# Kernel optimization log

Hardware: AMD Instinct MI355X
Metric: run time of the kernel (lower is better)

Reference implementation:

```python
import jax, jax.numpy as jnp
import numpy as np

# SOM hyperparameters (match init_kwargs)
M, N = 64, 64
NODES = M * N
FEATS = 256
BATCH = 1024
LR = 0.5
RADIUS_FACTOR = 1.1
TOTAL_ITER = 100000
SIGMA = max(M, N) * RADIUS_FACTOR


def setup_inputs() -> dict:
    key = jax.random.key(0)
    k1, k2 = jax.random.split(key)
    x = jax.random.uniform(k1, (BATCH, FEATS), dtype=jnp.float32)
    map_w = jax.random.uniform(k2, (NODES, FEATS), dtype=jnp.float32)
    return {"x": x, "map_w": map_w, "iteration": 0}


def _grid_locs():
    ii, jj = jnp.meshgrid(jnp.arange(M), jnp.arange(N), indexing='ij')
    return jnp.stack([ii.ravel(), jj.ravel()], axis=1)  # (NODES, 2) int32


def reference(x, map_w, iteration):
    B = x.shape[0]
    # ---- feedforward: squared distances (B, NODES) via GEMM expansion,
    # avoiding the (B, NODES, FEATS) broadcast the TF code materializes.
    x2 = jnp.sum(x * x, axis=1, keepdims=True)          # (B, 1)
    w2 = jnp.sum(map_w * map_w, axis=1)                  # (NODES,)
    sqd = x2 + w2[None, :] - 2.0 * (x @ map_w.T)         # (B, NODES)
    bmu_indices = jnp.argmin(sqd, axis=1)                # (B,)

    # ---- backprop: neighborhood-weighted codebook update
    locs = _grid_locs()                                  # (NODES, 2)
    bmu_locs = locs[bmu_indices]                         # (B, 2)
    # grid distance^2 between every node and each sample's BMU: (B, NODES)
    d2 = jnp.sum((locs[None, :, :] - bmu_locs[:, None, :]) ** 2, axis=2).astype(jnp.float32)

    lambda_g = TOTAL_ITER / SIGMA
    decay = jnp.exp(jnp.float32(-float(iteration) / lambda_g))
    radius = SIGMA * decay + 1e-6
    lr = LR * decay

    impact = jnp.exp(-d2 / (2.0 * radius * radius))
    in_radius = (jnp.sqrt(d2) <= radius).astype(jnp.float32)
    lr_op = impact * in_radius * lr                      # (B, NODES)

    # weight_update[n,d] = sum_b lr_op[b,n] * (x[b,d] - map_w[n,d])
    # computed without the (B, NODES, FEATS) intermediate:
    upd = (jnp.einsum('bn,bd->nd', lr_op, x) - lr_op.sum(axis=0)[:, None] * map_w) / B
    new_map = map_w + upd
    return new_map, bmu_indices
```

## Files before the change

kernel.cpp:

```cpp
#include <hip/hip_runtime.h>
#include <math.h>

#define NODES 4096
#define FEATS 256
#define BATCH 1024
#define LR_C 0.5f
#define SIGMA_C 70.4f

typedef _Float16 f16x8 __attribute__((ext_vector_type(8)));
typedef float floatx4 __attribute__((ext_vector_type(4)));

__device__ __forceinline__ void get_params(int it, float& lr, float& r2, float& i2r2) {
    float decay = __expf(-(float)it * (SIGMA_C / 100000.0f));
    float radius = SIGMA_C * decay + 1e-6f;
    lr = LR_C * decay;
    r2 = radius * radius;
    i2r2 = 1.0f / (2.0f * r2);
}

__device__ __forceinline__ unsigned fkey(float f) {
    unsigned u = __float_as_uint(f);
    return (u & 0x80000000u) ? ~u : (u | 0x80000000u);
}
__device__ __forceinline__ unsigned long long shfl_xor_u64(unsigned long long v, int mask) {
    unsigned lo = (unsigned)v, hi = (unsigned)(v >> 32);
    lo = __shfl_xor(lo, mask, 64);
    hi = __shfl_xor(hi, mask, 64);
    return ((unsigned long long)hi << 32) | lo;
}

__global__ __launch_bounds__(256) void k_gemm1min(const float* __restrict__ X, const float* __restrict__ Wm,
                                                  unsigned long long* __restrict__ gmin) {
    __shared__ _Float16 Ah[128][40];
    __shared__ _Float16 Al[128][40];
    __shared__ _Float16 Bh[64][40];
    __shared__ _Float16 Bl[64][40];
    __shared__ float w2s[64];
    const int n0 = blockIdx.x * 64;
    const int b0 = blockIdx.y * 128;
    const int t = threadIdx.x;
    const int wave = t >> 6, lane = t & 63;
    const int lm = lane & 15, quad = lane >> 4;
    const int arow = t >> 1, ako = (t & 1) * 16;
    const int brow = t >> 2, bko = (t & 3) * 8;
    float w2p = 0.0f;
    floatx4 acc[2][4] = {};
    for (int k0 = 0; k0 < FEATS; k0 += 32) {
        {
            union { _Float16 h[16]; float4 q[2]; } uh, ul;
#pragma unroll
            for (int c = 0; c < 4; ++c) {
                float4 v = *(const float4*)&X[(size_t)(b0 + arow) * FEATS + k0 + ako + c * 4];
                _Float16 h0 = (_Float16)v.x, h1 = (_Float16)v.y, h2 = (_Float16)v.z, h3 = (_Float16)v.w;
                uh.h[c * 4 + 0] = h0; uh.h[c * 4 + 1] = h1; uh.h[c * 4 + 2] = h2; uh.h[c * 4 + 3] = h3;
                ul.h[c * 4 + 0] = (_Float16)(v.x - (float)h0);
                ul.h[c * 4 + 1] = (_Float16)(v.y - (float)h1);
                ul.h[c * 4 + 2] = (_Float16)(v.z - (float)h2);
                ul.h[c * 4 + 3] = (_Float16)(v.w - (float)h3);
            }
            *(float4*)&Ah[arow][ako] = uh.q[0];
            *(float4*)&Ah[arow][ako + 8] = uh.q[1];
            *(float4*)&Al[arow][ako] = ul.q[0];
            *(float4*)&Al[arow][ako + 8] = ul.q[1];
        }
        {
            union { _Float16 h[8]; float4 q; } uh, ul;
#pragma unroll
            for (int c = 0; c < 2; ++c) {
                float4 v = *(const float4*)&Wm[(size_t)(n0 + brow) * FEATS + k0 + bko + c * 4];
                w2p += v.x * v.x + v.y * v.y + v.z * v.z + v.w * v.w;
                _Float16 h0 = (_Float16)v.x, h1 = (_Float16)v.y, h2 = (_Float16)v.z, h3 = (_Float16)v.w;
                uh.h[c * 4 + 0] = h0; uh.h[c * 4 + 1] = h1; uh.h[c * 4 + 2] = h2; uh.h[c * 4 + 3] = h3;
                ul.h[c * 4 + 0] = (_Float16)(v.x - (float)h0);
                ul.h[c * 4 + 1] = (_Float16)(v.y - (float)h1);
                ul.h[c * 4 + 2] = (_Float16)(v.z - (float)h2);
                ul.h[c * 4 + 3] = (_Float16)(v.w - (float)h3);
            }
            *(float4*)&Bh[brow][bko] = uh.q;
            *(float4*)&Bl[brow][bko] = ul.q;
        }
        __syncthreads();
        f16x8 ah[2], al[2], bh[4], bl[4];
#pragma unroll
        for (int i = 0; i < 2; ++i) {
            ah[i] = *(f16x8*)&Ah[wave * 32 + i * 16 + lm][quad * 8];
            al[i] = *(f16x8*)&Al[wave * 32 + i * 16 + lm][quad * 8];
        }
#pragma unroll
        for (int j = 0; j < 4; ++j) {
            bh[j] = *(f16x8*)&Bh[j * 16 + lm][quad * 8];
            bl[j] = *(f16x8*)&Bl[j * 16 + lm][quad * 8];
        }
#pragma unroll
        for (int i = 0; i < 2; ++i)
#pragma unroll
            for (int j = 0; j < 4; ++j) {
                acc[i][j] = __builtin_amdgcn_mfma_f32_16x16x32_f16(ah[i], bh[j], acc[i][j], 0, 0, 0);
                acc[i][j] = __builtin_amdgcn_mfma_f32_16x16x32_f16(ah[i], bl[j], acc[i][j], 0, 0, 0);
                acc[i][j] = __builtin_amdgcn_mfma_f32_16x16x32_f16(al[i], bh[j], acc[i][j], 0, 0, 0);
            }
        __syncthreads();
    }
    w2p += __shfl_xor(w2p, 1, 64);
    w2p += __shfl_xor(w2p, 2, 64);
    if ((t & 3) == 0) w2s[brow] = w2p;
    __syncthreads();
#pragma unroll
    for (int i = 0; i < 2; ++i)
#pragma unroll
        for (int r = 0; r < 4; ++r) {
            const int row = b0 + wave * 32 + i * 16 + quad * 4 + r;
            unsigned long long m = 0xFFFFFFFFFFFFFFFFULL;
#pragma unroll
            for (int j = 0; j < 4; ++j) {
                float v = w2s[j * 16 + lm] - 2.0f * acc[i][j][r];
                unsigned long long k = ((unsigned long long)fkey(v) << 32) | (unsigned)(n0 + j * 16 + lm);
                if (k < m) m = k;
            }
#pragma unroll
            for (int mk = 1; mk < 16; mk <<= 1) {
                unsigned long long o = shfl_xor_u64(m, mk);
                if (o < m) m = o;
            }
            if (lm == 0) atomicMin(&gmin[row], m);
        }
}

__global__ __launch_bounds__(256) void k_lropX(const unsigned long long* __restrict__ gmin,
                                               const int* __restrict__ itp, const float* __restrict__ X,
                                               _Float16* __restrict__ lrT, float* __restrict__ Svec,
                                               _Float16* __restrict__ XT, float* __restrict__ out1) {
    const int blk = blockIdx.x;
    const int t = threadIdx.x;
    if (blk < 2048) {
        __shared__ int bmu_s[1024];
        __shared__ float texp[64];
        __shared__ float red4[4];
#pragma unroll
        for (int j = 0; j < 4; ++j)
            bmu_s[t + j * 256] = (int)(gmin[t + j * 256] & 0xFFFFFFFFULL);
        float lr, r2, i2r2;
        get_params(itp[0], lr, r2, i2r2);
        if (t < 64) texp[t] = __expf(-(float)(t * t) * i2r2);
        __syncthreads();
        if (blk < 4) out1[blk * 256 + t] = (float)bmu_s[blk * 256 + t];
        const int n = blk * 2 + (t >> 7);
        const int b0 = (t & 127) * 8;
        const int ni = n >> 6, nj = n & 63;
        float s = 0.0f;
        union { _Float16 h[8]; float4 q; } u;
#pragma unroll
        for (int c = 0; c < 8; ++c) {
            int m = bmu_s[b0 + c];
            int di = ni - (m >> 6); di = di < 0 ? -di : di;
            int dj = nj - (m & 63); dj = dj < 0 ? -dj : dj;
            int d2 = di * di + dj * dj;
            float val = ((float)d2 <= r2) ? lr * texp[di] * texp[dj] : 0.0f;
            u.h[c] = (_Float16)val;
            s += val;
        }
        *(float4*)&lrT[(size_t)n * BATCH + b0] = u.q;
        const int lane = t & 63, wave = t >> 6;
#pragma unroll
        for (int off = 32; off > 0; off >>= 1) s += __shfl_down(s, off, 64);
        if (lane == 0) red4[wave] = s;
        __syncthreads();
        if (t < 2) Svec[blk * 2 + t] = red4[2 * t] + red4[2 * t + 1];
    } else {
        __shared__ _Float16 T[64][72];
        const int blk2 = blk - 2048;
        const int b0 = (blk2 & 15) * 64, d0 = (blk2 >> 4) * 64;
        {
            const int bl = t >> 2, dq = (t & 3) * 16;
            union { _Float16 h[16]; } u;
#pragma unroll
            for (int c = 0; c < 4; ++c) {
                float4 v = *(const float4*)&X[(size_t)(b0 + bl) * FEATS + d0 + dq + c * 4];
                u.h[c * 4 + 0] = (_Float16)v.x; u.h[c * 4 + 1] = (_Float16)v.y;
                u.h[c * 4 + 2] = (_Float16)v.z; u.h[c * 4 + 3] = (_Float16)v.w;
            }
#pragma unroll
            for (int c = 0; c < 16; ++c) T[bl][dq + c] = u.h[c];
        }
        __syncthreads();
        {
            const int dl = t >> 2, bq = (t & 3) * 16;
            union { _Float16 h[16]; float4 q[2]; } u;
#pragma unroll
            for (int c = 0; c < 16; ++c) u.h[c] = T[bq + c][dl];
            *(float4*)&XT[(size_t)(d0 + dl) * BATCH + b0 + bq] = u.q[0];
            *(float4*)&XT[(size_t)(d0 + dl) * BATCH + b0 + bq + 8] = u.q[1];
        }
    }
}

__global__ __launch_bounds__(256) void k_gemm2c(const _Float16* __restrict__ lrT, const _Float16* __restrict__ XT,
                                                const float* __restrict__ Svec, const float* __restrict__ Wm,
                                                float* __restrict__ out0) {
    __shared__ _Float16 As[32][136];
    __shared__ _Float16 Bs[64][136];
    __shared__ float Svl[32];
    const int d0 = blockIdx.x * 64;
    const int n0 = blockIdx.y * 32;
    const int t = threadIdx.x;
    const int wave = t >> 6, lane = t & 63;
    const int wm = wave & 1, wn = wave >> 1;
    const int lm = lane & 15, quad = lane >> 4;
    if (t < 32) Svl[t] = Svec[n0 + t];
    const int arow = t >> 3, acoff = (t & 7) * 16;
    const int brow = t >> 2, bcoff = (t & 3) * 32;
    floatx4 acc0 = {}, acc1 = {};
    for (int k0 = 0; k0 < BATCH; k0 += 128) {
        *(float4*)&As[arow][acoff] = *(const float4*)&lrT[(size_t)(n0 + arow) * BATCH + k0 + acoff];
        *(float4*)&As[arow][acoff + 8] = *(const float4*)&lrT[(size_t)(n0 + arow) * BATCH + k0 + acoff + 8];
#pragma unroll
        for (int c = 0; c < 4; ++c)
            *(float4*)&Bs[brow][bcoff + c * 8] =
                *(const float4*)&XT[(size_t)(d0 + brow) * BATCH + k0 + bcoff + c * 8];
        __syncthreads();
#pragma unroll
        for (int ks = 0; ks < 128; ks += 32) {
            f16x8 a = *(f16x8*)&As[wm * 16 + lm][ks + quad * 8];
            f16x8 b0 = *(f16x8*)&Bs[wn * 32 + lm][ks + quad * 8];
            f16x8 b1 = *(f16x8*)&Bs[wn * 32 + 16 + lm][ks + quad * 8];
            acc0 = __builtin_amdgcn_mfma_f32_16x16x32_f16(a, b0, acc0, 0, 0, 0);
            acc1 = __builtin_amdgcn_mfma_f32_16x16x32_f16(a, b1, acc1, 0, 0, 0);
        }
        __syncthreads();
    }
    const float invB = 1.0f / (float)BATCH;
#pragma unroll
    for (int r = 0; r < 4; ++r) {
        int rowN = n0 + wm * 16 + quad * 4 + r;
        float cc = 1.0f - Svl[rowN - n0] * invB;
        int col0 = d0 + wn * 32 + lm;
        int col1 = col0 + 16;
        out0[(size_t)rowN * FEATS + col0] = Wm[(size_t)rowN * FEATS + col0] * cc + acc0[r] * invB;
        out0[(size_t)rowN * FEATS + col1] = Wm[(size_t)rowN * FEATS + col1] * cc + acc1[r] * invB;
    }
}

extern "C" void kernel_launch(void* const* d_in, const int* in_sizes, int n_in,
                              void* d_out, int out_size, void* d_ws, size_t ws_size,
                              hipStream_t stream) {
    const float* X = (const float*)d_in[0];
    const float* Wm = (const float*)d_in[1];
    const int* itp = (const int*)d_in[2];
    float* out0 = (float*)d_out;
    float* out1 = out0 + (size_t)NODES * FEATS;

    char* ws = (char*)d_ws;
    unsigned long long* gmin = (unsigned long long*)(ws + 0);
    float* Svec     = (float*)(ws + 8192);
    _Float16* XT    = (_Float16*)(ws + 24576);
    _Float16* lrT   = (_Float16*)(ws + 548864);

    hipMemsetAsync(gmin, 0xFF, 1024 * sizeof(unsigned long long), stream);
    k_gemm1min<<<dim3(64, 8), 256, 0, stream>>>(X, Wm, gmin);
    k_lropX<<<2112, 256, 0, stream>>>(gmin, itp, X, lrT, Svec, XT, out1);
    k_gemm2c<<<dim3(4, 128), 256, 0, stream>>>(lrT, XT, Svec, Wm, out0);
}
```

Measured before the change: 96.53 us.

## Fuse lr_op generation into second GEMM and move X transpose into first kernel

```diff
diff --git a/kernel.cpp b/kernel.cpp
--- a/kernel.cpp
+++ b/kernel.cpp
@@ -30,15 +30,44 @@
 }
 
 __global__ __launch_bounds__(256) void k_gemm1min(const float* __restrict__ X, const float* __restrict__ Wm,
-                                                  unsigned long long* __restrict__ gmin) {
+                                                  unsigned long long* __restrict__ gmin,
+                                                  _Float16* __restrict__ XT) {
+    const int t = threadIdx.x;
+    const int blk = blockIdx.x;
+    if (blk >= 512) {
+        __shared__ _Float16 T[64][72];
+        const int blk2 = blk - 512;
+        const int b0 = (blk2 & 15) * 64, d0 = (blk2 >> 4) * 64;
+        {
+            const int bl = t >> 2, dq = (t & 3) * 16;
+            _Float16 h[16];
+#pragma unroll
+            for (int c = 0; c < 4; ++c) {
+                float4 v = *(const float4*)&X[(size_t)(b0 + bl) * FEATS + d0 + dq + c * 4];
+                h[c * 4 + 0] = (_Float16)v.x; h[c * 4 + 1] = (_Float16)v.y;
+                h[c * 4 + 2] = (_Float16)v.z; h[c * 4 + 3] = (_Float16)v.w;
+            }
+#pragma unroll
+            for (int c = 0; c < 16; ++c) T[bl][dq + c] = h[c];
+        }
+        __syncthreads();
+        {
+            const int dl = t >> 2, bq = (t & 3) * 16;
+            union { _Float16 h[16]; float4 q[2]; } u;
+#pragma unroll
+            for (int c = 0; c < 16; ++c) u.h[c] = T[bq + c][dl];
+            *(float4*)&XT[(size_t)(d0 + dl) * BATCH + b0 + bq] = u.q[0];
+            *(float4*)&XT[(size_t)(d0 + dl) * BATCH + b0 + bq + 8] = u.q[1];
+        }
+        return;
+    }
     __shared__ _Float16 Ah[128][40];
     __shared__ _Float16 Al[128][40];
     __shared__ _Float16 Bh[64][40];
     __shared__ _Float16 Bl[64][40];
     __shared__ float w2s[64];
-    const int n0 = blockIdx.x * 64;
-    const int b0 = blockIdx.y * 128;
-    const int t = threadIdx.x;
+    const int n0 = (blk & 63) * 64;
+    const int b0 = (blk >> 6) * 128;
     const int wave = t >> 6, lane = t & 63;
     const int lm = lane & 15, quad = lane >> 4;
     const int arow = t >> 1, ako = (t & 1) * 16;
@@ -126,117 +155,82 @@
         }
 }
 
-__global__ __launch_bounds__(256) void k_lropX(const unsigned long long* __restrict__ gmin,
-                                               const int* __restrict__ itp, const float* __restrict__ X,
-                                               _Float16* __restrict__ lrT, float* __restrict__ Svec,
-                                               _Float16* __restrict__ XT, float* __restrict__ out1) {
+__global__ __launch_bounds__(256) void k_gemm2d(const unsigned long long* __restrict__ gmin,
+                                                const int* __restrict__ itp,
+                                                const _Float16* __restrict__ XT,
+                                                const float* __restrict__ Wm,
+                                                float* __restrict__ out0, float* __restrict__ out1) {
+    __shared__ _Float16 As[16][1032];
+    __shared__ _Float16 T2h[4096];
+    __shared__ int bmu_s[1024];
+    __shared__ float Sv[16];
+    const int t = threadIdx.x;
     const int blk = blockIdx.x;
-    const int t = threadIdx.x;
-    if (blk < 2048) {
-        __shared__ int bmu_s[1024];
-        __shared__ float texp[64];
-        __shared__ float red4[4];
-#pragma unroll
-        for (int j = 0; j < 4; ++j)
-            bmu_s[t + j * 256] = (int)(gmin[t + j * 256] & 0xFFFFFFFFULL);
-        float lr, r2, i2r2;
-        get_params(itp[0], lr, r2, i2r2);
-        if (t < 64) texp[t] = __expf(-(float)(t * t) * i2r2);
-        __syncthreads();
-        if (blk < 4) out1[blk * 256 + t] = (float)bmu_s[blk * 256 + t];
-        const int n = blk * 2 + (t >> 7);
-        const int b0 = (t & 127) * 8;
-        const int ni = n >> 6, nj = n & 63;
+    const int n0 = blk * 16;
+    float lr, r2, i2r2;
+    get_params(itp[0], lr, r2, i2r2);
+#pragma unroll
+    for (int i = 0; i < 4; ++i) bmu_s[t * 4 + i] = (int)(gmin[t * 4 + i] & 0xFFFFFFFFULL);
+#pragma unroll
+    for (int i = 0; i < 16; ++i) {
+        int e = t * 16 + i;
+        int di = e >> 6, dj = e & 63;
+        int d2 = di * di + dj * dj;
+        float val = ((float)d2 <= r2) ? lr * __expf(-(float)d2 * i2r2) : 0.0f;
+        T2h[e] = (_Float16)val;
+    }
+    if (t < 16) Sv[t] = 0.0f;
+    __syncthreads();
+    if (blk < 4) out1[blk * 256 + t] = (float)bmu_s[blk * 256 + t];
+    {
+        const int node_l = t & 15;
+        const int kb = (t >> 4) * 64;
+        const int node = n0 + node_l;
+        const int ni = node >> 6, nj = node & 63;
         float s = 0.0f;
-        union { _Float16 h[8]; float4 q; } u;
-#pragma unroll
-        for (int c = 0; c < 8; ++c) {
-            int m = bmu_s[b0 + c];
-            int di = ni - (m >> 6); di = di < 0 ? -di : di;
-            int dj = nj - (m & 63); dj = dj < 0 ? -dj : dj;
-            int d2 = di * di + dj * dj;
-            float val = ((float)d2 <= r2) ? lr * texp[di] * texp[dj] : 0.0f;
-            u.h[c] = (_Float16)val;
-            s += val;
-        }
-        *(float4*)&lrT[(size_t)n * BATCH + b0] = u.q;
-        const int lane = t & 63, wave = t >> 6;
-#pragma unroll
-        for (int off = 32; off > 0; off >>= 1) s += __shfl_down(s, off, 64);
-        if (lane == 0) red4[wave] = s;
-        __syncthreads();
-        if (t < 2) Svec[blk * 2 + t] = red4[2 * t] + red4[2 * t + 1];
-    } else {
-        __shared__ _Float16 T[64][72];
-        const int blk2 = blk - 2048;
-        const int b0 = (blk2 & 15) * 64, d0 = (blk2 >> 4) * 64;
-        {
-            const int bl = t >> 2, dq = (t & 3) * 16;
-            union { _Float16 h[16]; } u;
-#pragma unroll
-            for (int c = 0; c < 4; ++c) {
-                float4 v = *(const float4*)&X[(size_t)(b0 + bl) * FEATS + d0 + dq + c * 4];
-                u.h[c * 4 + 0] = (_Float16)v.x; u.h[c * 4 + 1] = (_Float16)v.y;
-                u.h[c * 4 + 2] = (_Float16)v.z; u.h[c * 4 + 3] = (_Float16)v.w;
-            }
-#pragma unroll
-            for (int c = 0; c < 16; ++c) T[bl][dq + c] = u.h[c];
-        }
-        __syncthreads();
-        {
-            const int dl = t >> 2, bq = (t & 3) * 16;
-            union { _Float16 h[16]; float4 q[2]; } u;
-#pragma unroll
-            for (int c = 0; c < 16; ++c) u.h[c] = T[bq + c][dl];
-            *(float4*)&XT[(size_t)(d0 + dl) * BATCH + b0 + bq] = u.q[0];
-            *(float4*)&XT[(size_t)(d0 + dl) * BATCH + b0 + bq + 8] = u.q[1];
-        }
-    }
-}
-
-__global__ __launch_bounds__(256) void k_gemm2c(const _Float16* __restrict__ lrT, const _Float16* __restrict__ XT,
-                                                const float* __restrict__ Svec, const float* __restrict__ Wm,
-                                                float* __restrict__ out0) {
-    __shared__ _Float16 As[32][136];
-    __shared__ _Float16 Bs[64][136];
-    __shared__ float Svl[32];
-    const int d0 = blockIdx.x * 64;
-    const int n0 = blockIdx.y * 32;
-    const int t = threadIdx.x;
+#pragma unroll
+        for (int g = 0; g < 8; ++g) {
+            union { _Float16 h[8]; f16x8 v; } u;
+#pragma unroll
+            for (int e = 0; e < 8; ++e) {
+                int m = bmu_s[kb + g * 8 + e];
+                int di = ni - (m >> 6); di = di < 0 ? -di : di;
+                int dj = nj - (m & 63); dj = dj < 0 ? -dj : dj;
+                _Float16 h = T2h[di * 64 + dj];
+                u.h[e] = h;
+                s += (float)h;
+            }
+            *(f16x8*)&As[node_l][kb + g * 8] = u.v;
+        }
+        atomicAdd(&Sv[node_l], s);
+    }
+    __syncthreads();
     const int wave = t >> 6, lane = t & 63;
-    const int wm = wave & 1, wn = wave >> 1;
     const int lm = lane & 15, quad = lane >> 4;
-    if (t < 32) Svl[t] = Svec[n0 + t];
-    const int arow = t >> 3, acoff = (t & 7) * 16;
-    const int brow = t >> 2, bcoff = (t & 3) * 32;
-    floatx4 acc0 = {}, acc1 = {};
-    for (int k0 = 0; k0 < BATCH; k0 += 128) {
-        *(float4*)&As[arow][acoff] = *(const float4*)&lrT[(size_t)(n0 + arow) * BATCH + k0 + acoff];
-        *(float4*)&As[arow][acoff + 8] = *(const float4*)&lrT[(size_t)(n0 + arow) * BATCH + k0 + acoff + 8];
-#pragma unroll
-        for (int c = 0; c < 4; ++c)
-            *(float4*)&Bs[brow][bcoff + c * 8] =
-                *(const float4*)&XT[(size_t)(d0 + brow) * BATCH + k0 + bcoff + c * 8];
-        __syncthreads();
-#pragma unroll
-        for (int ks = 0; ks < 128; ks += 32) {
-            f16x8 a = *(f16x8*)&As[wm * 16 + lm][ks + quad * 8];
-            f16x8 b0 = *(f16x8*)&Bs[wn * 32 + lm][ks + quad * 8];
-            f16x8 b1 = *(f16x8*)&Bs[wn * 32 + 16 + lm][ks + quad * 8];
-            acc0 = __builtin_amdgcn_mfma_f32_16x16x32_f16(a, b0, acc0, 0, 0, 0);
-            acc1 = __builtin_amdgcn_mfma_f32_16x16x32_f16(a, b1, acc1, 0, 0, 0);
-        }
-        __syncthreads();
+    const int dbase = wave * 64;
+    floatx4 acc[4] = {};
+    const _Float16* xt0 = XT + (size_t)(dbase + lm) * BATCH + quad * 8;
+#pragma unroll 4
+    for (int c = 0; c < 32; ++c) {
+        const int k0 = c * 32;
+        f16x8 a = *(f16x8*)&As[lm][k0 + quad * 8];
+#pragma unroll
+        for (int j = 0; j < 4; ++j) {
+            f16x8 b = *(const f16x8*)&xt0[(size_t)(j * 16) * BATCH + k0];
+            acc[j] = __builtin_amdgcn_mfma_f32_16x16x32_f16(a, b, acc[j], 0, 0, 0);
+        }
     }
     const float invB = 1.0f / (float)BATCH;
 #pragma unroll
-    for (int r = 0; r < 4; ++r) {
-        int rowN = n0 + wm * 16 + quad * 4 + r;
-        float cc = 1.0f - Svl[rowN - n0] * invB;
-        int col0 = d0 + wn * 32 + lm;
-        int col1 = col0 + 16;
-        out0[(size_t)rowN * FEATS + col0] = Wm[(size_t)rowN * FEATS + col0] * cc + acc0[r] * invB;
-        out0[(size_t)rowN * FEATS + col1] = Wm[(size_t)rowN * FEATS + col1] * cc + acc1[r] * invB;
+    for (int j = 0; j < 4; ++j) {
+        const int col = dbase + j * 16 + lm;
+#pragma unroll
+        for (int r = 0; r < 4; ++r) {
+            const int nr = quad * 4 + r;
+            const float cc = 1.0f - Sv[nr] * invB;
+            out0[(size_t)(n0 + nr) * FEATS + col] =
+                Wm[(size_t)(n0 + nr) * FEATS + col] * cc + acc[j][r] * invB;
+        }
     }
 }
 
@@ -251,12 +245,9 @@
 
     char* ws = (char*)d_ws;
     unsigned long long* gmin = (unsigned long long*)(ws + 0);
-    float* Svec     = (float*)(ws + 8192);
-    _Float16* XT    = (_Float16*)(ws + 24576);
-    _Float16* lrT   = (_Float16*)(ws + 548864);
+    _Float16* XT = (_Float16*)(ws + 8192);
 
     hipMemsetAsync(gmin, 0xFF, 1024 * sizeof(unsigned long long), stream);
-    k_gemm1min<<<dim3(64, 8), 256, 0, stream>>>(X, Wm, gmin);
-    k_lropX<<<2112, 256, 0, stream>>>(gmin, itp, X, lrT, Svec, XT, out1);
-    k_gemm2c<<<dim3(4, 128), 256, 0, stream>>>(lrT, XT, Svec, Wm, out0);
-}
+    k_gemm1min<<<576, 256, 0, stream>>>(X, Wm, gmin, XT);
+    k_gemm2d<<<256, 256, 0, stream>>>(gmin, itp, XT, Wm, out0, out1);
+}
```

Result: slower. 99.23 us (+2.8%).
